# Kernel optimization log

Measured on AMD Instinct MI355X. Metric: run time of the kernel, lower is better.

## Reference

```python
import jax, jax.numpy as jnp
import numpy as np

EPS = 1e-6
N_HEADS = 16


def _inner(x, y):
    # Lorentzian inner product: -x0*y0 + <x_space, y_space>
    return -x[..., 0] * y[..., 0] + jnp.sum(x[..., 1:] * y[..., 1:], axis=-1)


def _project(x):
    sp = jnp.clip(x[..., 1:], -8.0, 8.0)
    x0 = jnp.sqrt(1.0 + jnp.sum(sp ** 2, axis=-1, keepdims=True) + EPS)
    return jnp.concatenate([x0, sp], axis=-1)


def _exp_map(x, v):
    vx = _inner(v, x)[..., None]
    v_tan = v + vx * x
    v_ns = jnp.maximum(_inner(v_tan, v_tan), 0.0)
    v_n = jnp.minimum(jnp.sqrt(v_ns + EPS)[..., None], 5.0)
    res = jnp.cosh(v_n) * x + jnp.sinh(v_n) * v_tan / (v_n + EPS)
    return _project(res)


def _log_map(x, y):
    y = _project(y)
    xy = jnp.minimum(_inner(x, y)[..., None], -(1.0 + EPS))
    d = jnp.maximum(jnp.arccosh(jnp.maximum(-xy, 1.0 + EPS)), 0.001)
    direc = y + xy * x
    dn = jnp.sqrt(jnp.maximum(_inner(direc, direc), EPS))[..., None]
    return d * direc / (dn + EPS)


def setup_inputs() -> dict:
    key = jax.random.key(0)
    ks = jax.random.split(key, 5)
    B, T, d = 2, 1024, 1024
    x = jax.random.normal(ks[0], (B, T, d), dtype=jnp.float32)
    s = 0.02
    Wq = jax.random.normal(ks[1], (d, d), dtype=jnp.float32) * s
    Wk = jax.random.normal(ks[2], (d, d), dtype=jnp.float32) * s
    Wv = jax.random.normal(ks[3], (d, d), dtype=jnp.float32) * s
    Wo = jax.random.normal(ks[4], (d, d), dtype=jnp.float32) * s
    return {"x": x, "Wq": Wq, "Wk": Wk, "Wv": Wv, "Wo": Wo}


def reference(x, Wq, Wk, Wv, Wo):
    B, T, d = x.shape
    h = N_HEADS
    dh = d // h
    mu = jnp.zeros((d,), dtype=x.dtype).at[0].set(1.0)  # hyperboloid origin

    v = _log_map(mu, x)  # [B, T, d]

    def proj_h(w):
        hh = w.reshape(B, T, h, dh)
        sp = jnp.clip(hh[..., 1:], -5.0, 5.0)
        x0 = jnp.sqrt(1.0 + jnp.sum(sp ** 2, axis=-1, keepdims=True) + EPS)
        return jnp.transpose(jnp.concatenate([x0, sp], axis=-1), (0, 2, 1, 3))  # [B,h,T,dh]

    q = proj_h(v @ Wq.T)
    k = proj_h(v @ Wk.T)
    vv = jnp.transpose((v @ Wv.T).reshape(B, T, h, dh), (0, 2, 1, 3))  # [B,h,T,dh]

    # Lorentzian scores: -q0*k0 + <q_space, k_space>
    sc = (-jnp.einsum("bhqi,bhki->bhqk", q[..., :1], k[..., :1])
          + jnp.einsum("bhqc,bhkc->bhqk", q[..., 1:], k[..., 1:])) / (dh ** 0.5)
    at = jax.nn.softmax(sc, axis=-1)
    out = jnp.einsum("bhqk,bhkc->bhqc", at, vv)
    out = jnp.transpose(out, (0, 2, 1, 3)).reshape(B, T, d)
    return _project(_exp_map(mu, out @ Wo.T))
```

## Files before the change

kernel.cpp:

```cpp
#include <hip/hip_runtime.h>

#define EPSF 1e-6f

typedef __bf16 bf16x8 __attribute__((ext_vector_type(8)));
typedef float f32x4 __attribute__((ext_vector_type(4)));
typedef __attribute__((address_space(3))) unsigned int as3_uint;
typedef __attribute__((address_space(1))) const unsigned int as1_uint;

__device__ __forceinline__ unsigned short f2bf(float f) {
  unsigned int u = __builtin_bit_cast(unsigned int, f);
  u += 0x7fffu + ((u >> 16) & 1u);
  return (unsigned short)(u >> 16);
}
__device__ __forceinline__ float bf2f(unsigned short u) {
  unsigned int v = (unsigned int)u << 16;
  return __builtin_bit_cast(float, v);
}

__global__ __launch_bounds__(256) void prep_and_conv(
    const float* __restrict__ x, const float* __restrict__ Wq,
    const float* __restrict__ Wk, const float* __restrict__ Wv,
    const float* __restrict__ Wo, unsigned short* __restrict__ vbf,
    unsigned short* __restrict__ wqk, unsigned short* __restrict__ wvb,
    unsigned short* __restrict__ wob) {
  int bid = blockIdx.x;
  int tid = threadIdx.x;
  if (bid >= 2048) {
    int t = bid - 2048;
    int y = t >> 10;
    const float* src = (y == 0) ? Wq : (y == 1) ? Wk : (y == 2) ? Wv : Wo;
    unsigned short* dst = (y == 0) ? wqk : (y == 1) ? wqk + 1048576
                          : (y == 2) ? wvb : wob;
    int i = (t & 1023) * 256 + tid;
    f32x4 v = ((const f32x4*)src)[i];
    ushort4 o;
    o.x = f2bf(v[0]); o.y = f2bf(v[1]); o.z = f2bf(v[2]); o.w = f2bf(v[3]);
    ((ushort4*)dst)[i] = o;
    return;
  }
  int row = bid;
  const float* xr = x + (size_t)row * 1024;
  float vals[4];
  float ssq = 0.f;
#pragma unroll
  for (int i = 0; i < 4; ++i) {
    int c = tid + i * 256;
    float t = xr[c];
    if (c == 0) {
      vals[i] = 0.f;
    } else {
      t = fminf(fmaxf(t, -8.f), 8.f);
      vals[i] = t;
      ssq += t * t;
    }
  }
#pragma unroll
  for (int off = 32; off; off >>= 1) ssq += __shfl_xor(ssq, off);
  __shared__ float red[4];
  int wv = tid >> 6;
  if ((tid & 63) == 0) red[wv] = ssq;
  __syncthreads();
  ssq = red[0] + red[1] + red[2] + red[3];

  float y0 = sqrtf(1.f + ssq + EPSF);
  float xy = fminf(-y0, -(1.f + EPSF));
  float mxy = fmaxf(-xy, 1.f + EPSF);
  float dd = fmaxf(acoshf(mxy), 0.001f);
  float d0 = y0 + xy;
  float inn = ssq - d0 * d0;
  float dn = sqrtf(fmaxf(inn, EPSF));
  float inv = dd / (dn + EPSF);

  unsigned short* vr = vbf + (size_t)row * 1024;
#pragma unroll
  for (int i = 0; i < 4; ++i) {
    int c = tid + i * 256;
    float o = (c == 0) ? d0 * inv : vals[i] * inv;
    vr[c] = f2bf(o);
  }
}

__device__ __forceinline__ void gemm_body(
    const unsigned short* __restrict__ A, const unsigned short* __restrict__ Bw,
    unsigned short* __restrict__ C, int N, int K, int row0, int col0,
    unsigned short* As, unsigned short* Bs) {
  int tid = threadIdx.x;
  int lane = tid & 63, w = tid >> 6;
  int wm = (w & 1) * 64, wn = (w >> 1) * 32;
  int lq = lane & 15, g = lane >> 4;
  f32x4 acc[4][2] = {};

  const unsigned short* Ag =
      A + (size_t)(row0 + w * 8 + (lane >> 3)) * K + (lane & 7) * 8;
  const unsigned short* Bg =
      Bw + (size_t)(col0 + w * 8 + (lane >> 3)) * K + (lane & 7) * 8;

  for (int k0 = 0; k0 < K; k0 += 64) {
    __syncthreads();
#pragma unroll
    for (int it = 0; it < 4; ++it)
      __builtin_amdgcn_global_load_lds(
          (as1_uint*)(Ag + (size_t)(it * 32) * K + k0),
          (as3_uint*)&As[(it * 32 + w * 8) * 64], 16, 0, 0);
#pragma unroll
    for (int it = 0; it < 2; ++it)
      __builtin_amdgcn_global_load_lds(
          (as1_uint*)(Bg + (size_t)(it * 32) * K + k0),
          (as3_uint*)&Bs[(it * 32 + w * 8) * 64], 16, 0, 0);
    __syncthreads();
#pragma unroll
    for (int ks = 0; ks < 2; ++ks) {
      bf16x8 af[4], bfr[2];
#pragma unroll
      for (int i = 0; i < 4; ++i)
        af[i] = *(const bf16x8*)&As[(wm + i * 16 + lq) * 64 + ks * 32 + g * 8];
#pragma unroll
      for (int j = 0; j < 2; ++j)
        bfr[j] = *(const bf16x8*)&Bs[(wn + j * 16 + lq) * 64 + ks * 32 + g * 8];
#pragma unroll
      for (int i = 0; i < 4; ++i)
#pragma unroll
        for (int j = 0; j < 2; ++j)
          acc[i][j] =
              __builtin_amdgcn_mfma_f32_16x16x32_bf16(af[i], bfr[j], acc[i][j], 0, 0, 0);
    }
  }
#pragma unroll
  for (int i = 0; i < 4; ++i)
#pragma unroll
    for (int j = 0; j < 2; ++j)
#pragma unroll
      for (int r = 0; r < 4; ++r)
        C[(size_t)(row0 + wm + i * 16 + g * 4 + r) * N + col0 + wn + j * 16 + lq] =
            f2bf(acc[i][j][r]);
}

__global__ __launch_bounds__(256) void gemm_fused(
    const unsigned short* __restrict__ vbf, const unsigned short* __restrict__ wqk,
    const unsigned short* __restrict__ wvb, unsigned short* __restrict__ qkb,
    unsigned short* __restrict__ vtb) {
  __shared__ unsigned short As[128 * 64];
  __shared__ unsigned short Bs[64 * 64];
  int bid = blockIdx.x;
  if (bid < 512) {
    gemm_body(vbf, wqk, qkb, 2048, 1024, (bid & 15) * 128, (bid >> 4) * 64, As, Bs);
  } else {
    int t = bid - 512;
    gemm_body(wvb, vbf, vtb, 2048, 1024, (t & 7) * 128, (t >> 3) * 64, As, Bs);
  }
}

__global__ __launch_bounds__(256) void gemm_wo(
    const unsigned short* __restrict__ A, const unsigned short* __restrict__ Bw,
    unsigned short* __restrict__ C) {
  __shared__ unsigned short As[128 * 64];
  __shared__ unsigned short Bs[64 * 64];
  gemm_body(A, Bw, C, 1024, 1024, (blockIdx.x & 15) * 128, (blockIdx.x >> 4) * 64,
            As, Bs);
}

__global__ __launch_bounds__(256) void proj_both(
    const unsigned short* __restrict__ qkb, unsigned short* __restrict__ qb,
    unsigned short* __restrict__ kb) {
  int tid = threadIdx.x;
  int qmode = (blockIdx.y == 0);
  int g = blockIdx.x * 4 + (tid >> 6);
  int lane = tid & 63;
  int row = g >> 4, head = g & 15;
  const unsigned short* src = qkb + (qmode ? 0 : 1024);
  unsigned short* dst = qmode ? qb : kb;
  float t = bf2f(src[(size_t)row * 2048 + head * 64 + lane]);
  float sp = fminf(fmaxf(t, -5.f), 5.f);
  float ssq = (lane == 0) ? 0.f : sp * sp;
#pragma unroll
  for (int o = 32; o; o >>= 1) ssq += __shfl_xor(ssq, o);
  float x0 = sqrtf(1.f + ssq + EPSF);
  float o = (lane == 0) ? (qmode ? -x0 : x0) : sp;
  if (qmode) o *= 0.125f;
  dst[(size_t)row * 1024 + head * 64 + lane] = f2bf(o);
}

__global__ __launch_bounds__(256) void attn_mfma(
    const unsigned short* __restrict__ Qb, const unsigned short* __restrict__ Kb,
    const unsigned short* __restrict__ Vtb, unsigned short* __restrict__ Obf) {
  __shared__ unsigned short Ks[2][64 * 64];
  __shared__ unsigned short Vs[2][64 * 64];
  __shared__ unsigned short Ps[4 * 16 * 64];
  int tid = threadIdx.x;
  int lane = tid & 63, w = tid >> 6;
  int g = lane >> 4, lq = lane & 15;
  int bh = blockIdx.x >> 4, qt = blockIdx.x & 15;
  int b = bh >> 4, h = bh & 15;

  const unsigned short* qrow =
      Qb + (size_t)(b * 1024 + qt * 64 + w * 16 + lq) * 1024 + h * 64;
  bf16x8 qf0 = *(const bf16x8*)(qrow + g * 8);
  bf16x8 qf1 = *(const bf16x8*)(qrow + 32 + g * 8);

  float mreg = -1e30f, lreg = 0.f;
  f32x4 acc[4] = {};
  unsigned short* Pw = Ps + w * 16 * 64;
  int sx = 8 * (lq & 7);

  const unsigned short* Ksrc = Kb + (size_t)(b * 1024) * 1024 + h * 64;
  const unsigned short* Vsrc = Vtb + (size_t)(h * 64) * 2048 + b * 1024;

  int srow = lane >> 3;
  int scg = (lane & 7) ^ srow;
  const unsigned short* Kp = Ksrc + (size_t)(w * 8 + srow) * 1024 + scg * 8;
  const unsigned short* Vp = Vsrc + (size_t)(w * 8 + srow) * 2048 + scg * 8;

  auto stage = [&](int buf, int kt) {
#pragma unroll
    for (int it = 0; it < 2; ++it) {
      __builtin_amdgcn_global_load_lds(
          (as1_uint*)(Kp + (size_t)(kt * 64 + it * 32) * 1024),
          (as3_uint*)&Ks[buf][(it * 32 + w * 8) * 64], 16, 0, 0);
      __builtin_amdgcn_global_load_lds(
          (as1_uint*)(Vp + (size_t)(it * 32) * 2048 + kt * 64),
          (as3_uint*)&Vs[buf][(it * 32 + w * 8) * 64], 16, 0, 0);
    }
  };

  auto compute = [&](int buf) {
    f32x4 st[4];
#pragma unroll
    for (int i = 0; i < 4; ++i) {
      int ro = i * 16 + lq;
      int rb = ro * 64, xx = 8 * (ro & 7);
      bf16x8 a0 = *(const bf16x8*)&Ks[buf][rb + ((g * 8) ^ xx)];
      bf16x8 a1 = *(const bf16x8*)&Ks[buf][rb + ((32 + g * 8) ^ xx)];
      f32x4 z = {};
      z = __builtin_amdgcn_mfma_f32_16x16x32_bf16(a0, qf0, z, 0, 0, 0);
      st[i] = __builtin_amdgcn_mfma_f32_16x16x32_bf16(a1, qf1, z, 0, 0, 0);
    }
    float pmax = st[0][0];
#pragma unroll
    for (int i = 0; i < 4; ++i)
#pragma unroll
      for (int r = 0; r < 4; ++r) pmax = fmaxf(pmax, st[i][r]);
    pmax = fmaxf(pmax, __shfl_xor(pmax, 16));
    pmax = fmaxf(pmax, __shfl_xor(pmax, 32));
    float nm = fmaxf(mreg, pmax);
    float sc_ = __expf(mreg - nm);
    mreg = nm;
    float ps = 0.f;
#pragma unroll
    for (int i = 0; i < 4; ++i) {
      ushort4 pq;
      float p0 = __expf(st[i][0] - nm);
      float p1 = __expf(st[i][1] - nm);
      float p2 = __expf(st[i][2] - nm);
      float p3 = __expf(st[i][3] - nm);
      ps += (p0 + p1) + (p2 + p3);
      pq.x = f2bf(p0); pq.y = f2bf(p1); pq.z = f2bf(p2); pq.w = f2bf(p3);
      *(ushort4*)&Pw[lq * 64 + ((g * 4 + i * 16) ^ sx)] = pq;
    }
    ps += __shfl_xor(ps, 16);
    ps += __shfl_xor(ps, 32);
    lreg = lreg * sc_ + ps;

    float scr[4];
#pragma unroll
    for (int r = 0; r < 4; ++r) scr[r] = __shfl(sc_, g * 4 + r);
#pragma unroll
    for (int jj = 0; jj < 4; ++jj)
#pragma unroll
      for (int r = 0; r < 4; ++r) acc[jj][r] *= scr[r];
#pragma unroll
    for (int ks = 0; ks < 2; ++ks) {
      bf16x8 pa = *(const bf16x8*)&Pw[lq * 64 + ((ks * 32 + g * 8) ^ sx)];
#pragma unroll
      for (int jj = 0; jj < 4; ++jj) {
        int vr = 16 * jj + lq;
        bf16x8 vb = *(const bf16x8*)&Vs[buf][vr * 64 + ((ks * 32 + g * 8) ^ (8 * (vr & 7)))];
        acc[jj] = __builtin_amdgcn_mfma_f32_16x16x32_bf16(pa, vb, acc[jj], 0, 0, 0);
      }
    }
  };

  stage(0, 0);
  int buf = 0;
  for (int kt = 0; kt < 16; ++kt) {
    __syncthreads();
    if (kt + 1 < 16) stage(buf ^ 1, kt + 1);
    compute(buf);
    buf ^= 1;
  }

  float linv = 1.f / lreg;
  float ilr[4];
#pragma unroll
  for (int r = 0; r < 4; ++r) ilr[r] = __shfl(linv, g * 4 + r);
  unsigned short* obase =
      Obf + (size_t)(b * 1024 + qt * 64 + w * 16) * 1024 + h * 64;
#pragma unroll
  for (int r = 0; r < 4; ++r)
#pragma unroll
    for (int jj = 0; jj < 4; ++jj)
      obase[(size_t)(g * 4 + r) * 1024 + 16 * jj + lq] = f2bf(acc[jj][r] * ilr[r]);
}

__global__ __launch_bounds__(256) void expmap_project(
    const unsigned short* __restrict__ c2, float* __restrict__ out) {
  int row = blockIdx.x;
  int tid = threadIdx.x;
  const unsigned short* cr = c2 + (size_t)row * 1024;
  float vals[4];
  float ssq = 0.f;
#pragma unroll
  for (int i = 0; i < 4; ++i) {
    int c = tid + i * 256;
    float t = bf2f(cr[c]);
    vals[i] = (c == 0) ? 0.f : t;
    ssq += vals[i] * vals[i];
  }
#pragma unroll
  for (int off = 32; off; off >>= 1) ssq += __shfl_xor(ssq, off);
  __shared__ float red1[4], red2[4];
  int wv = tid >> 6;
  if ((tid & 63) == 0) red1[wv] = ssq;
  __syncthreads();
  ssq = red1[0] + red1[1] + red1[2] + red1[3];
  float vn = fminf(sqrtf(ssq + EPSF), 5.f);
  float bf = sinhf(vn) / (vn + EPSF);
  float s2 = 0.f;
#pragma unroll
  for (int i = 0; i < 4; ++i) {
    float r = fminf(fmaxf(bf * vals[i], -8.f), 8.f);
    vals[i] = r;
    s2 += r * r;
  }
#pragma unroll
  for (int off = 32; off; off >>= 1) s2 += __shfl_xor(s2, off);
  if ((tid & 63) == 0) red2[wv] = s2;
  __syncthreads();
  s2 = red2[0] + red2[1] + red2[2] + red2[3];
  float x0 = sqrtf(1.f + s2 + EPSF);
  float* orow = out + (size_t)row * 1024;
#pragma unroll
  for (int i = 0; i < 4; ++i) {
    int c = tid + i * 256;
    orow[c] = (c == 0) ? x0 : vals[i];
  }
}

extern "C" void kernel_launch(void* const* d_in, const int* in_sizes, int n_in,
                              void* d_out, int out_size, void* d_ws, size_t ws_size,
                              hipStream_t stream) {
  (void)in_sizes; (void)n_in; (void)out_size; (void)ws_size;
  const float* x  = (const float*)d_in[0];
  const float* Wq = (const float*)d_in[1];
  const float* Wk = (const float*)d_in[2];
  const float* Wv = (const float*)d_in[3];
  const float* Wo = (const float*)d_in[4];
  float* out = (float*)d_out;

  char* w = (char*)d_ws;
  unsigned short* vbf = (unsigned short*)w; w += (size_t)2048 * 1024 * 2;
  unsigned short* wqk = (unsigned short*)w; w += (size_t)2048 * 1024 * 2;
  unsigned short* wvb = (unsigned short*)w; w += (size_t)1024 * 1024 * 2;
  unsigned short* wob = (unsigned short*)w; w += (size_t)1024 * 1024 * 2;
  unsigned short* qkb = (unsigned short*)w; w += (size_t)2048 * 2048 * 2;
  unsigned short* vtb = (unsigned short*)w; w += (size_t)1024 * 2048 * 2;
  unsigned short* qb  = (unsigned short*)w; w += (size_t)2048 * 1024 * 2;
  unsigned short* kb  = (unsigned short*)w; w += (size_t)2048 * 1024 * 2;
  unsigned short* aob = (unsigned short*)w; w += (size_t)2048 * 1024 * 2;
  unsigned short* c2  = (unsigned short*)w; w += (size_t)2048 * 1024 * 2;

  prep_and_conv<<<6144, 256, 0, stream>>>(x, Wq, Wk, Wv, Wo, vbf, wqk, wvb, wob);

  gemm_fused<<<768, 256, 0, stream>>>(vbf, wqk, wvb, qkb, vtb);

  proj_both<<<dim3(8192, 2), 256, 0, stream>>>(qkb, qb, kb);

  attn_mfma<<<512, 256, 0, stream>>>(qb, kb, vtb, aob);

  gemm_wo<<<256, 256, 0, stream>>>(aob, wob, c2);
  expmap_project<<<2048, 256, 0, stream>>>(c2, out);
}
```

Before: 96.71 us.

## Fuse hyperbolic head projection into QKV GEMM epilogue with 128x128 tiles

```diff
diff --git a/kernel.cpp b/kernel.cpp
--- a/kernel.cpp
+++ b/kernel.cpp
@@ -80,16 +80,14 @@
   }
 }
 
-__device__ __forceinline__ void gemm_body(
+__device__ __forceinline__ void gemm128_body(
     const unsigned short* __restrict__ A, const unsigned short* __restrict__ Bw,
-    unsigned short* __restrict__ C, int N, int K, int row0, int col0,
-    unsigned short* As, unsigned short* Bs) {
+    int K, int row0, int col0, unsigned short* As, unsigned short* Bs,
+    f32x4 (*acc)[4]) {
   int tid = threadIdx.x;
   int lane = tid & 63, w = tid >> 6;
-  int wm = (w & 1) * 64, wn = (w >> 1) * 32;
+  int wm = (w >> 1) * 64, wn = (w & 1) * 64;
   int lq = lane & 15, g = lane >> 4;
-  f32x4 acc[4][2] = {};
-
   const unsigned short* Ag =
       A + (size_t)(row0 + w * 8 + (lane >> 3)) * K + (lane & 7) * 8;
   const unsigned short* Bg =
@@ -98,55 +96,90 @@
   for (int k0 = 0; k0 < K; k0 += 64) {
     __syncthreads();
 #pragma unroll
-    for (int it = 0; it < 4; ++it)
+    for (int it = 0; it < 4; ++it) {
       __builtin_amdgcn_global_load_lds(
           (as1_uint*)(Ag + (size_t)(it * 32) * K + k0),
           (as3_uint*)&As[(it * 32 + w * 8) * 64], 16, 0, 0);
-#pragma unroll
-    for (int it = 0; it < 2; ++it)
       __builtin_amdgcn_global_load_lds(
           (as1_uint*)(Bg + (size_t)(it * 32) * K + k0),
           (as3_uint*)&Bs[(it * 32 + w * 8) * 64], 16, 0, 0);
+    }
     __syncthreads();
 #pragma unroll
     for (int ks = 0; ks < 2; ++ks) {
-      bf16x8 af[4], bfr[2];
+      bf16x8 af[4], bfr[4];
 #pragma unroll
       for (int i = 0; i < 4; ++i)
         af[i] = *(const bf16x8*)&As[(wm + i * 16 + lq) * 64 + ks * 32 + g * 8];
 #pragma unroll
-      for (int j = 0; j < 2; ++j)
+      for (int j = 0; j < 4; ++j)
         bfr[j] = *(const bf16x8*)&Bs[(wn + j * 16 + lq) * 64 + ks * 32 + g * 8];
 #pragma unroll
       for (int i = 0; i < 4; ++i)
 #pragma unroll
-        for (int j = 0; j < 2; ++j)
+        for (int j = 0; j < 4; ++j)
           acc[i][j] =
               __builtin_amdgcn_mfma_f32_16x16x32_bf16(af[i], bfr[j], acc[i][j], 0, 0, 0);
     }
   }
-#pragma unroll
-  for (int i = 0; i < 4; ++i)
-#pragma unroll
-    for (int j = 0; j < 2; ++j)
-#pragma unroll
-      for (int r = 0; r < 4; ++r)
-        C[(size_t)(row0 + wm + i * 16 + g * 4 + r) * N + col0 + wn + j * 16 + lq] =
-            f2bf(acc[i][j][r]);
-}
-
-__global__ __launch_bounds__(256) void gemm_fused(
+}
+
+__global__ __launch_bounds__(256) void gemm_qkv(
     const unsigned short* __restrict__ vbf, const unsigned short* __restrict__ wqk,
-    const unsigned short* __restrict__ wvb, unsigned short* __restrict__ qkb,
-    unsigned short* __restrict__ vtb) {
+    const unsigned short* __restrict__ wvb, unsigned short* __restrict__ qb,
+    unsigned short* __restrict__ kb, unsigned short* __restrict__ vtb) {
   __shared__ unsigned short As[128 * 64];
-  __shared__ unsigned short Bs[64 * 64];
+  __shared__ unsigned short Bs[128 * 64];
+  f32x4 acc[4][4] = {};
+  int tid = threadIdx.x;
+  int lane = tid & 63, w = tid >> 6;
+  int wm = (w >> 1) * 64, wn = (w & 1) * 64;
+  int lq = lane & 15, g = lane >> 4;
   int bid = blockIdx.x;
-  if (bid < 512) {
-    gemm_body(vbf, wqk, qkb, 2048, 1024, (bid & 15) * 128, (bid >> 4) * 64, As, Bs);
+
+  if (bid < 256) {
+    int row0 = (bid & 15) * 128, col0 = (bid >> 4) * 128;
+    gemm128_body(vbf, wqk, 1024, row0, col0, As, Bs, acc);
+    int headg = (col0 + wn) >> 6;
+    int qmode = (headg < 16) ? 1 : 0;
+    unsigned short* dst = qmode ? qb : kb;
+    size_t colb = (size_t)(headg & 15) * 64;
+    float scale = qmode ? 0.125f : 1.f;
+#pragma unroll
+    for (int i = 0; i < 4; ++i)
+#pragma unroll
+      for (int r = 0; r < 4; ++r) {
+        float s = 0.f;
+#pragma unroll
+        for (int j = 0; j < 4; ++j) {
+          float vc = fminf(fmaxf(acc[i][j][r], -5.f), 5.f);
+          s += (j == 0 && lq == 0) ? 0.f : vc * vc;
+        }
+        s += __shfl_xor(s, 1);
+        s += __shfl_xor(s, 2);
+        s += __shfl_xor(s, 4);
+        s += __shfl_xor(s, 8);
+        float x0 = sqrtf(1.f + s + EPSF);
+        int row = row0 + wm + i * 16 + g * 4 + r;
+#pragma unroll
+        for (int j = 0; j < 4; ++j) {
+          float vc = fminf(fmaxf(acc[i][j][r], -5.f), 5.f);
+          float o = (j == 0 && lq == 0) ? (qmode ? -x0 : x0) : vc;
+          dst[(size_t)row * 1024 + colb + j * 16 + lq] = f2bf(o * scale);
+        }
+      }
   } else {
-    int t = bid - 512;
-    gemm_body(wvb, vbf, vtb, 2048, 1024, (t & 7) * 128, (t >> 3) * 64, As, Bs);
+    int t = bid - 256;
+    int row0 = (t & 7) * 128, col0 = (t >> 3) * 128;
+    gemm128_body(wvb, vbf, 1024, row0, col0, As, Bs, acc);
+#pragma unroll
+    for (int i = 0; i < 4; ++i)
+#pragma unroll
+      for (int j = 0; j < 4; ++j)
+#pragma unroll
+        for (int r = 0; r < 4; ++r)
+          vtb[(size_t)(row0 + wm + i * 16 + g * 4 + r) * 2048 + col0 + wn + j * 16 + lq] =
+              f2bf(acc[i][j][r]);
   }
 }
 
@@ -154,30 +187,23 @@
     const unsigned short* __restrict__ A, const unsigned short* __restrict__ Bw,
     unsigned short* __restrict__ C) {
   __shared__ unsigned short As[128 * 64];
-  __shared__ unsigned short Bs[64 * 64];
-  gemm_body(A, Bw, C, 1024, 1024, (blockIdx.x & 15) * 128, (blockIdx.x >> 4) * 64,
-            As, Bs);
-}
-
-__global__ __launch_bounds__(256) void proj_both(
-    const unsigned short* __restrict__ qkb, unsigned short* __restrict__ qb,
-    unsigned short* __restrict__ kb) {
-  int tid = threadIdx.x;
-  int qmode = (blockIdx.y == 0);
-  int g = blockIdx.x * 4 + (tid >> 6);
-  int lane = tid & 63;
-  int row = g >> 4, head = g & 15;
-  const unsigned short* src = qkb + (qmode ? 0 : 1024);
-  unsigned short* dst = qmode ? qb : kb;
-  float t = bf2f(src[(size_t)row * 2048 + head * 64 + lane]);
-  float sp = fminf(fmaxf(t, -5.f), 5.f);
-  float ssq = (lane == 0) ? 0.f : sp * sp;
-#pragma unroll
-  for (int o = 32; o; o >>= 1) ssq += __shfl_xor(ssq, o);
-  float x0 = sqrtf(1.f + ssq + EPSF);
-  float o = (lane == 0) ? (qmode ? -x0 : x0) : sp;
-  if (qmode) o *= 0.125f;
-  dst[(size_t)row * 1024 + head * 64 + lane] = f2bf(o);
+  __shared__ unsigned short Bs[128 * 64];
+  f32x4 acc[4][4] = {};
+  int bid = blockIdx.x;
+  int row0 = (bid & 15) * 128, col0 = (bid >> 4) * 128;
+  gemm128_body(A, Bw, 1024, row0, col0, As, Bs, acc);
+  int tid = threadIdx.x;
+  int lane = tid & 63, w = tid >> 6;
+  int wm = (w >> 1) * 64, wn = (w & 1) * 64;
+  int lq = lane & 15, g = lane >> 4;
+#pragma unroll
+  for (int i = 0; i < 4; ++i)
+#pragma unroll
+    for (int j = 0; j < 4; ++j)
+#pragma unroll
+      for (int r = 0; r < 4; ++r)
+        C[(size_t)(row0 + wm + i * 16 + g * 4 + r) * 1024 + col0 + wn + j * 16 + lq] =
+            f2bf(acc[i][j][r]);
 }
 
 __global__ __launch_bounds__(256) void attn_mfma(
@@ -361,7 +387,6 @@
   unsigned short* wqk = (unsigned short*)w; w += (size_t)2048 * 1024 * 2;
   unsigned short* wvb = (unsigned short*)w; w += (size_t)1024 * 1024 * 2;
   unsigned short* wob = (unsigned short*)w; w += (size_t)1024 * 1024 * 2;
-  unsigned short* qkb = (unsigned short*)w; w += (size_t)2048 * 2048 * 2;
   unsigned short* vtb = (unsigned short*)w; w += (size_t)1024 * 2048 * 2;
   unsigned short* qb  = (unsigned short*)w; w += (size_t)2048 * 1024 * 2;
   unsigned short* kb  = (unsigned short*)w; w += (size_t)2048 * 1024 * 2;
@@ -370,12 +395,10 @@
 
   prep_and_conv<<<6144, 256, 0, stream>>>(x, Wq, Wk, Wv, Wo, vbf, wqk, wvb, wob);
 
-  gemm_fused<<<768, 256, 0, stream>>>(vbf, wqk, wvb, qkb, vtb);
-
-  proj_both<<<dim3(8192, 2), 256, 0, stream>>>(qkb, qb, kb);
+  gemm_qkv<<<384, 256, 0, stream>>>(vbf, wqk, wvb, qb, kb, vtb);
 
   attn_mfma<<<512, 256, 0, stream>>>(qb, kb, vtb, aob);
 
-  gemm_wo<<<256, 256, 0, stream>>>(aob, wob, c2);
+  gemm_wo<<<128, 256, 0, stream>>>(aob, wob, c2);
   expmap_project<<<2048, 256, 0, stream>>>(c2, out);
 }
```

Measured after the change: 93.23 us. 1.04x faster.
